# Kernel optimization log

Hardware: AMD Instinct MI355X
Metric: run time of the kernel (lower is better)

## Reference

```python
import jax, jax.numpy as jnp
import numpy as np

HEAD_DIM = 64
SELECT = 256  # number of selected rows/cols (m)
NUM_ITER = 4  # Newton-Schulz iterations


def _select_idx(T, mask, m):
    # top-k over sum of features (select_type='sum'), done under stop_gradient (torch.no_grad)
    somme = jax.lax.stop_gradient(jnp.sum(T, axis=-1))  # [B,H,N]
    neg = -jnp.finfo(somme.dtype).max
    somme = jnp.where(mask[:, None, :], somme, neg)
    _, idx = jax.lax.top_k(somme, m)  # [B,H,m], descending like argsort(descending=True)[:m]
    return idx


def _gather_rows(T, idx):
    # T: [B,H,N,D], idx: [B,H,m] -> [B,H,m,D]  (index_select over flattened (b h n))
    return jnp.take_along_axis(T, idx[..., None], axis=2)


def _iterative_inv(mat, num_iter):
    m = mat.shape[-1]
    I = jnp.eye(m, dtype=mat.dtype)
    K = mat
    # V0 = K^T / max_j(sum_i K_ij)
    scale = 1.0 / jnp.max(jnp.sum(K, axis=-2), axis=-1)[:, :, None, None]
    V = scale * jnp.swapaxes(K, -1, -2)
    for _ in range(num_iter):
        KV = jnp.matmul(K, V)
        V = jnp.matmul(0.25 * V, 13.0 * I - jnp.matmul(KV, 15.0 * I - jnp.matmul(KV, 7.0 * I - KV)))
    return V


def setup_inputs() -> dict:
    key = jax.random.key(0)
    kq, kk, kv = jax.random.split(key, 3)
    B, H, N, D = 2, 8, 4096, HEAD_DIM
    Q = jax.random.normal(kq, (B, H, N, D), dtype=jnp.float32)
    K = jax.random.normal(kk, (B, H, N, D), dtype=jnp.float32)
    V = jax.random.normal(kv, (B, H, N, D), dtype=jnp.float32)
    mask = jnp.ones((B, N), dtype=bool)
    return {"Q": Q, "K": K, "V": V, "mask": mask}


def reference(Q, K, V, mask):
    m = SELECT
    Qs = Q / np.sqrt(HEAD_DIM).astype(np.float32)
    # select_mode='default' -> index_select_different: indices for K from K, for Q from (scaled) Q
    idx_k = _select_idx(K, mask, m)
    idx_q = _select_idx(Qs, mask, m)
    nc = _gather_rows(K, idx_k)   # [B,H,m,D] selected columns (from K)
    nr = _gather_rows(Qs, idx_k := idx_q if False else idx_q) if False else _gather_rows(Qs, idx_q)  # [B,H,m,D]
    c = jnp.einsum('bhnd,bhmd->bhnm', Qs, nc)   # [B,H,N,m]
    r = jnp.einsum('bhmd,bhnd->bhmn', nr, K)    # [B,H,m,N]
    neg = -jnp.finfo(Qs.dtype).max
    r = jnp.where(mask[:, None, None, :], r, neg)
    kernel_1 = jax.nn.softmax(c, axis=-1)                 # [B,H,N,m]
    u = _gather_rows(kernel_1, idx_q)                     # [B,H,m,m]
    kernel_3 = jax.nn.softmax(r, axis=-1)                 # [B,H,m,N]
    kernel_2_inv = _iterative_inv(u, NUM_ITER)            # [B,H,m,m]
    RV = jnp.matmul(kernel_3, V)                          # [B,H,m,D]
    X = jnp.matmul(kernel_1, jnp.matmul(kernel_2_inv, RV))  # [B,H,N,D]
    return X
```

## Files before the change

### kernel.cpp

```cpp
#include <hip/hip_runtime.h>
#include <float.h>


#define G    16
#define NSEQ 4096
#define DH   64
#define MSEL 256
#define NSL  16

typedef __attribute__((ext_vector_type(8))) short short8;
typedef __attribute__((ext_vector_type(4))) float floatx4;
typedef __attribute__((ext_vector_type(4))) unsigned short ushort4v;
typedef unsigned short ush;

static __device__ __forceinline__ ush f2b(float x) {
    union { float f; unsigned u; } c{x};
    unsigned r = c.u + 0x7FFFu + ((c.u >> 16) & 1u);
    return (ush)(r >> 16);
}
static __device__ __forceinline__ float b2f(ush h) {
    union { unsigned u; float f; } c{(unsigned)h << 16};
    return c.f;
}
static __device__ __forceinline__ void split_store(ush* __restrict__ h, ush* __restrict__ l,
                                                   int off, float4 v, float scale) {
    float a0 = v.x * scale, a1 = v.y * scale, a2 = v.z * scale, a3 = v.w * scale;
    ush h0 = f2b(a0), h1 = f2b(a1), h2 = f2b(a2), h3 = f2b(a3);
    ushort4v hv = { h0, h1, h2, h3 };
    ushort4v lv = { f2b(a0 - b2f(h0)), f2b(a1 - b2f(h1)), f2b(a2 - b2f(h2)), f2b(a3 - b2f(h3)) };
    *(ushort4v*)&h[off] = hv;
    *(ushort4v*)&l[off] = lv;
}
static __device__ __forceinline__ floatx4 mfma3(short8 ah, short8 al, short8 bh, short8 bl, floatx4 acc) {
    acc = __builtin_amdgcn_mfma_f32_16x16x32_bf16(al, bh, acc, 0, 0, 0);
    acc = __builtin_amdgcn_mfma_f32_16x16x32_bf16(ah, bl, acc, 0, 0, 0);
    acc = __builtin_amdgcn_mfma_f32_16x16x32_bf16(ah, bh, acc, 0, 0, 0);
    return acc;
}

__global__ __launch_bounds__(256) void rowsum_kernel(const float* __restrict__ Q, const float* __restrict__ K,
                                                     float* __restrict__ sumQ, float* __restrict__ sumK,
                                                     float* __restrict__ k2) {
    long row = (long)blockIdx.x * 16 + (threadIdx.x >> 4);
    int c4 = (threadIdx.x & 15) * 4;
    float4 q = *(const float4*)(Q + row * DH + c4);
    float4 k = *(const float4*)(K + row * DH + c4);
    float qs = q.x + q.y + q.z + q.w;
    float ks = k.x + k.y + k.z + k.w;
    float k2s = k.x * k.x + k.y * k.y + k.z * k.z + k.w * k.w;
#pragma unroll
    for (int off = 8; off; off >>= 1) {
        qs += __shfl_xor(qs, off); ks += __shfl_xor(ks, off); k2s += __shfl_xor(k2s, off);
    }
    if ((threadIdx.x & 15) == 0) { sumQ[row] = qs; sumK[row] = ks; k2[row] = k2s; }
}

__global__ __launch_bounds__(256) void topk_select(const float* __restrict__ sumQ, const float* __restrict__ sumK,
                                                   int* __restrict__ idxQ, int* __restrict__ idxK,
                                                   const float* __restrict__ k2, float* __restrict__ Kmax2,
                                                   float* __restrict__ colsum) {
    __shared__ unsigned red[4];
    __shared__ float redf[4];
    __shared__ unsigned eqpre[64];
    __shared__ unsigned cnt_sel;
    int g = blockIdx.x, which = blockIdx.y;
    const float* s = (which ? sumK : sumQ) + (long)g * NSEQ;
    int* out = (which ? idxK : idxQ) + g * MSEL;
    int t = threadIdx.x, lane = t & 63, wid = t >> 6;
    if (which == 0) colsum[g * 256 + t] = 0.f;
    unsigned k[16];
#pragma unroll
    for (int i = 0; i < 16; i++) {
        unsigned u = __float_as_uint(s[t + 256 * i]);
        k[i] = (u & 0x80000000u) ? ~u : (u | 0x80000000u);
    }
    unsigned T = 0;
    for (int b = 31; b >= 0; b--) {
        unsigned trial = T | (1u << b);
        int c = 0;
#pragma unroll
        for (int i = 0; i < 16; i++) c += (k[i] >= trial);
#pragma unroll
        for (int off = 32; off; off >>= 1) c += __shfl_xor(c, off);
        __syncthreads();
        if (lane == 0) red[wid] = (unsigned)c;
        __syncthreads();
        unsigned tot = red[0] + red[1] + red[2] + red[3];
        if (tot == MSEL) { T = trial; break; }
        if (tot > MSEL) T = trial;
    }
    int cg = 0;
#pragma unroll
    for (int i = 0; i < 16; i++) cg += (k[i] > T);
#pragma unroll
    for (int off = 32; off; off >>= 1) cg += __shfl_xor(cg, off);
    __syncthreads();
    if (lane == 0) red[wid] = (unsigned)cg;
    if (t == 0) cnt_sel = 0;
    __syncthreads();
    unsigned ngreater = red[0] + red[1] + red[2] + red[3];
    unsigned want_eq = MSEL - ngreater;
#pragma unroll
    for (int i = 0; i < 16; i++) {
        unsigned long long be = __ballot(k[i] == T);
        if (lane == 0) eqpre[i * 4 + wid] = (unsigned)__popcll(be);
    }
    __syncthreads();
    if (t == 0) {
        unsigned run = 0;
        for (int j = 0; j < 64; j++) { unsigned c = eqpre[j]; eqpre[j] = run; run += c; }
    }
    __syncthreads();
#pragma unroll
    for (int i = 0; i < 16; i++) {
        int idx = t + 256 * i;
        unsigned long long lt = (1ull << lane) - 1;
        bool gt = (k[i] > T);
        unsigned long long bg = __ballot(gt);
        unsigned wbase = 0;
        if (lane == 0) wbase = atomicAdd(&cnt_sel, (unsigned)__popcll(bg));
        wbase = __shfl((int)wbase, 0);
        if (gt) out[wbase + __popcll(bg & lt)] = idx;
        bool eq = (k[i] == T);
        unsigned long long be = __ballot(eq);
        if (eq) {
            unsigned rank = eqpre[i * 4 + wid] + (unsigned)__popcll(be & lt);
            if (rank < want_eq) out[ngreater + rank] = idx;
        }
    }
    if (which == 1) {
        float mx = 0.f;
#pragma unroll
        for (int i = 0; i < 16; i++) mx = fmaxf(mx, k2[(long)g * NSEQ + t + 256 * i]);
#pragma unroll
        for (int off = 32; off; off >>= 1) mx = fmaxf(mx, __shfl_xor(mx, off));
        __syncthreads();
        if (lane == 0) redf[wid] = mx;
        __syncthreads();
        if (t == 0) Kmax2[g] = fmaxf(fmaxf(redf[0], redf[1]), fmaxf(redf[2], redf[3]));
    }
}

__global__ __launch_bounds__(256) void gather_kernel(const float* __restrict__ Q, const float* __restrict__ K,
                                                     const int* __restrict__ idxQ, const int* __restrict__ idxK,
                                                     const float* __restrict__ Kmax2,
                                                     float* __restrict__ nr,
                                                     ush* __restrict__ ncH, ush* __restrict__ ncL,
                                                     float* __restrict__ Mb) {
    int wid = threadIdx.x >> 6, lane = threadIdx.x & 63;
    long t = (long)blockIdx.x * 4 + wid;
    long g = t >> 8;
    int iq = idxQ[t], ik = idxK[t];
    float qv = Q[(g * NSEQ + iq) * DH + lane] * 0.125f;
    nr[t * DH + lane] = qv;
    float kv = K[(g * NSEQ + ik) * DH + lane];
    ush h = f2b(kv);
    ncH[t * DH + lane] = h;
    ncL[t * DH + lane] = f2b(kv - b2f(h));
    float n2 = qv * qv;
#pragma unroll
    for (int off = 32; off; off >>= 1) n2 += __shfl_xor(n2, off);
    if (lane == 0) Mb[t] = sqrtf(n2 * Kmax2[g]);
}

__global__ __launch_bounds__(256, 4) void flash_rv(const float* __restrict__ nr, const float* __restrict__ K,
                                                   const float* __restrict__ V, const float* __restrict__ Mb,
                                                   float* __restrict__ Lp, float* __restrict__ RVp) {
    __shared__ __align__(16) ush B1h[64 * 72];
    __shared__ __align__(16) ush B1l[64 * 72];
    __shared__ __align__(16) ush Ph[64 * 72];
    __shared__ float msh[64];
    __shared__ float lred[64][2];
    int ns = blockIdx.x, s = blockIdx.y, g = blockIdx.z;
    int t = threadIdx.x, lane = t & 63, w = t >> 6;
    int wr = w >> 1, wc = w & 1, ml = lane & 15, quad = lane >> 4;
    int lr = t >> 2, lq = t & 3;
    const float* nrg = nr + (long)g * 16384 + (long)s * 64 * 64;
    const float* Kg  = K + (long)g * 262144 + (long)ns * 256 * 64;
    const float* Vg  = V + (long)g * 262144 + (long)ns * 256 * 64;
    short8 Ah[2][2], Al[2][2];
#pragma unroll
    for (int i2 = 0; i2 < 2; i2++)
#pragma unroll
        for (int kq = 0; kq < 2; kq++) {
            const float* p = nrg + (wr * 32 + i2 * 16 + ml) * 64 + kq * 32 + quad * 8;
            float4 f0 = *(const float4*)p;
            float4 f1 = *(const float4*)(p + 4);
            float vals[8] = { f0.x, f0.y, f0.z, f0.w, f1.x, f1.y, f1.z, f1.w };
            short8 hh, ll;
#pragma unroll
            for (int j = 0; j < 8; j++) {
                ush h = f2b(vals[j]);
                hh[j] = (short)h;
                ll[j] = (short)f2b(vals[j] - b2f(h));
            }
            Ah[i2][kq] = hh; Al[i2][kq] = ll;
        }
    if (t < 64) msh[t] = Mb[g * 256 + s * 64 + t];
    float lsum[2][4] = {};
    floatx4 acc[2][2] = {};
    int vn = t >> 2, vdq = (t & 3) * 16;
    for (int it = 0; it < 4; it++) {
        __syncthreads();
        float4 kv[4], vv[4];
#pragma unroll
        for (int q = 0; q < 4; q++) kv[q] = *(const float4*)(Kg + (long)(it * 64 + lr) * 64 + lq * 16 + q * 4);
#pragma unroll
        for (int q = 0; q < 4; q++) vv[q] = *(const float4*)(Vg + (long)(it * 64 + vn) * 64 + vdq + q * 4);
#pragma unroll
        for (int q = 0; q < 4; q++) split_store(B1h, B1l, lr * 72 + lq * 16 + q * 4, kv[q], 1.0f);
        __syncthreads();
        floatx4 sa[2][2] = {};
#pragma unroll
        for (int kq = 0; kq < 2; kq++) {
            short8 b0h = *(const short8*)&B1h[(wc * 32 + ml) * 72 + kq * 32 + quad * 8];
            short8 b0l = *(const short8*)&B1l[(wc * 32 + ml) * 72 + kq * 32 + quad * 8];
            short8 b1h = *(const short8*)&B1h[(wc * 32 + 16 + ml) * 72 + kq * 32 + quad * 8];
            short8 b1l = *(const short8*)&B1l[(wc * 32 + 16 + ml) * 72 + kq * 32 + quad * 8];
            sa[0][0] = mfma3(Ah[0][kq], Al[0][kq], b0h, b0l, sa[0][0]);
            sa[0][1] = mfma3(Ah[0][kq], Al[0][kq], b1h, b1l, sa[0][1]);
            sa[1][0] = mfma3(Ah[1][kq], Al[1][kq], b0h, b0l, sa[1][0]);
            sa[1][1] = mfma3(Ah[1][kq], Al[1][kq], b1h, b1l, sa[1][1]);
        }
        __syncthreads();
#pragma unroll
        for (int i2 = 0; i2 < 2; i2++)
#pragma unroll
            for (int r = 0; r < 4; r++) {
                int row = wr * 32 + i2 * 16 + quad * 4 + r;
                float M = msh[row];
                float p0 = __expf(sa[i2][0][r] - M);
                float p1 = __expf(sa[i2][1][r] - M);
                lsum[i2][r] += p0 + p1;
                Ph[row * 72 + wc * 32 + ml] = f2b(p0);
                Ph[row * 72 + wc * 32 + 16 + ml] = f2b(p1);
            }
#pragma unroll
        for (int q = 0; q < 4; q++)
#pragma unroll
            for (int c = 0; c < 4; c++) {
                int d = vdq + q * 4 + c;
                int addr = d * 72 + ((((vn >> 3) ^ ((d >> 4) & 3)) << 3) | (vn & 7));
                B1h[addr] = f2b((&vv[q].x)[c]);
            }
        __syncthreads();
#pragma unroll
        for (int kq = 0; kq < 2; kq++) {
            short8 a0 = *(const short8*)&Ph[(wr * 32 + ml) * 72 + kq * 32 + quad * 8];
            short8 a1 = *(const short8*)&Ph[(wr * 32 + 16 + ml) * 72 + kq * 32 + quad * 8];
            int nb = kq * 4 + quad;
            short8 b0 = *(const short8*)&B1h[(wc * 32 + ml) * 72 + ((nb ^ (2 * wc)) << 3)];
            short8 b1 = *(const short8*)&B1h[(wc * 32 + 16 + ml) * 72 + ((nb ^ (2 * wc + 1)) << 3)];
            acc[0][0] = __builtin_amdgcn_mfma_f32_16x16x32_bf16(a0, b0, acc[0][0], 0, 0, 0);
            acc[0][1] = __builtin_amdgcn_mfma_f32_16x16x32_bf16(a0, b1, acc[0][1], 0, 0, 0);
            acc[1][0] = __builtin_amdgcn_mfma_f32_16x16x32_bf16(a1, b0, acc[1][0], 0, 0, 0);
            acc[1][1] = __builtin_amdgcn_mfma_f32_16x16x32_bf16(a1, b1, acc[1][1], 0, 0, 0);
        }
    }
#pragma unroll
    for (int i2 = 0; i2 < 2; i2++)
#pragma unroll
        for (int r = 0; r < 4; r++) {
            float v = lsum[i2][r];
#pragma unroll
            for (int off = 8; off; off >>= 1) v += __shfl_xor(v, off);
            if (ml == 0) lred[wr * 32 + i2 * 16 + quad * 4 + r][wc] = v;
        }
    __syncthreads();
    long p = ((long)(g * 4 + s)) * NSL + ns;
    if (t < 64) Lp[p * 64 + t] = lred[t][0] + lred[t][1];
    float* rvp = RVp + p * 4096;
#pragma unroll
    for (int i2 = 0; i2 < 2; i2++)
#pragma unroll
        for (int j2 = 0; j2 < 2; j2++)
#pragma unroll
            for (int r = 0; r < 4; r++)
                rvp[(wr * 32 + i2 * 16 + quad * 4 + r) * 64 + wc * 32 + j2 * 16 + ml] = acc[i2][j2][r];
}

template <int MODE>
__global__ __launch_bounds__(256, 4) void fused_cx(const float* __restrict__ A,
                                                   const ush* __restrict__ ncH, const ush* __restrict__ ncL,
                                                   const ush* __restrict__ WtH, const ush* __restrict__ WtL,
                                                   float* __restrict__ Out, float* __restrict__ colsum,
                                                   float ascale) {
    __shared__ __align__(16) ush SM[18432];
    ush* Ah = SM;            ush* Al = SM + 4608;
    ush* Bh = SM + 9216;     ush* Bl = SM + 13824;
    ush* Ph = SM;            ush* Pl = SM + 4608;
    ush* Wh = SM + 9216;     ush* Wl = SM + 13824;
    __shared__ float pm[256], ps[256], Mr[64], Lr[64];
    int strip = blockIdx.x, g = blockIdx.y;
    int t = threadIdx.x, lane = t & 63, w = t >> 6;
    int wr = w >> 1, wc = w & 1, ml = lane & 15, quad = lane >> 4;
    int lr = t >> 2, lq = t & 3;
    long aRows = (MODE == 0) ? 4096 : 256;
    const float* Ag = A + (long)g * aRows * 64 + (long)strip * 64 * 64;
    const ush* ncHg = ncH + (long)g * 16384;
    const ush* ncLg = ncL + (long)g * 16384;
#pragma unroll
    for (int q = 0; q < 4; q++) {
        float4 v = *(const float4*)(Ag + lr * 64 + lq * 16 + q * 4);
        split_store(Ah, Al, lr * 72 + lq * 16 + q * 4, v, ascale);
    }
    floatx4 sacc[4][4] = {};
    for (int c = 0; c < 4; c++) {
        __syncthreads();
        {
            const ush* sH = ncHg + (c * 64 + lr) * 64;
            const ush* sL = ncLg + (c * 64 + lr) * 64;
            *(uint4*)&Bh[lr * 72 + lq * 8]       = *(const uint4*)&sH[lq * 8];
            *(uint4*)&Bh[lr * 72 + (lq + 4) * 8] = *(const uint4*)&sH[(lq + 4) * 8];
            *(uint4*)&Bl[lr * 72 + lq * 8]       = *(const uint4*)&sL[lq * 8];
            *(uint4*)&Bl[lr * 72 + (lq + 4) * 8] = *(const uint4*)&sL[(lq + 4) * 8];
        }
        __syncthreads();
#pragma unroll
        for (int kq = 0; kq < 2; kq++) {
            short8 bh = *(const short8*)&Bh[(w * 16 + ml) * 72 + kq * 32 + quad * 8];
            short8 bl = *(const short8*)&Bl[(w * 16 + ml) * 72 + kq * 32 + quad * 8];
#pragma unroll
            for (int i = 0; i < 4; i++) {
                short8 afh = *(const short8*)&Ah[(16 * i + ml) * 72 + kq * 32 + quad * 8];
                short8 afl = *(const short8*)&Al[(16 * i + ml) * 72 + kq * 32 + quad * 8];
                sacc[c][i] = mfma3(afh, afl, bh, bl, sacc[c][i]);
            }
        }
    }
#pragma unroll
    for (int i = 0; i < 4; i++)
#pragma unroll
        for (int r = 0; r < 4; r++) {
            float mx = fmaxf(fmaxf(sacc[0][i][r], sacc[1][i][r]), fmaxf(sacc[2][i][r], sacc[3][i][r]));
#pragma unroll
            for (int off = 8; off; off >>= 1) mx = fmaxf(mx, __shfl_xor(mx, off));
            if (ml == 0) pm[(16 * i + quad * 4 + r) * 4 + w] = mx;
        }
    __syncthreads();
    if (t < 64) Mr[t] = fmaxf(fmaxf(pm[t * 4], pm[t * 4 + 1]), fmaxf(pm[t * 4 + 2], pm[t * 4 + 3]));
    __syncthreads();
#pragma unroll
    for (int i = 0; i < 4; i++)
#pragma unroll
        for (int r = 0; r < 4; r++) {
            int row = 16 * i + quad * 4 + r;
            float M = Mr[row];
            float sum = 0.f;
#pragma unroll
            for (int c = 0; c < 4; c++) {
                float p = __expf(sacc[c][i][r] - M);
                sacc[c][i][r] = p;
                sum += p;
            }
#pragma unroll
            for (int off = 8; off; off >>= 1) sum += __shfl_xor(sum, off);
            if (ml == 0) ps[row * 4 + w] = sum;
        }
    __syncthreads();
    if (t < 64) Lr[t] = ps[t * 4] + ps[t * 4 + 1] + ps[t * 4 + 2] + ps[t * 4 + 3];
    __syncthreads();
    if (MODE == 1) {
        float invL[4][4];
#pragma unroll
        for (int i = 0; i < 4; i++)
#pragma unroll
            for (int r = 0; r < 4; r++) invL[i][r] = 1.0f / Lr[16 * i + quad * 4 + r];
        float* ug = Out + (long)g * 65536 + (long)strip * 64 * 256;
#pragma unroll
        for (int i = 0; i < 4; i++)
#pragma unroll
            for (int r = 0; r < 4; r++) {
                int row = 16 * i + quad * 4 + r;
#pragma unroll
                for (int c = 0; c < 4; c++)
                    ug[(long)row * 256 + c * 64 + w * 16 + ml] = sacc[c][i][r] * invL[i][r];
            }
#pragma unroll
        for (int c = 0; c < 4; c++) {
            float v = 0.f;
#pragma unroll
            for (int i = 0; i < 4; i++)
#pragma unroll
                for (int r = 0; r < 4; r++) v += sacc[c][i][r] * invL[i][r];
            v += __shfl_xor(v, 16);
            v += __shfl_xor(v, 32);
            if (quad == 0) atomicAdd(&colsum[g * 256 + c * 64 + w * 16 + ml], v);
        }
        return;
    }
    floatx4 xacc[2][2] = {};
    const ush* wHg = WtH + (long)g * 16384;
    const ush* wLg = WtL + (long)g * 16384;
#pragma unroll
    for (int h = 0; h < 4; h++) {
        __syncthreads();
#pragma unroll
        for (int i = 0; i < 4; i++)
#pragma unroll
            for (int r = 0; r < 4; r++) {
                int row = 16 * i + quad * 4 + r;
                float p = sacc[h][i][r];
                ush hh = f2b(p);
                Ph[row * 72 + w * 16 + ml] = hh;
                Pl[row * 72 + w * 16 + ml] = f2b(p - b2f(hh));
            }
        {
            const ush* sH = wHg + lr * 256 + h * 64;
            const ush* sL = wLg + lr * 256 + h * 64;
            *(uint4*)&Wh[lr * 72 + lq * 8]       = *(const uint4*)&sH[lq * 8];
            *(uint4*)&Wh[lr * 72 + (lq + 4) * 8] = *(const uint4*)&sH[(lq + 4) * 8];
            *(uint4*)&Wl[lr * 72 + lq * 8]       = *(const uint4*)&sL[lq * 8];
            *(uint4*)&Wl[lr * 72 + (lq + 4) * 8] = *(const uint4*)&sL[(lq + 4) * 8];
        }
        __syncthreads();
#pragma unroll
        for (int kq = 0; kq < 2; kq++) {
            short8 a0h = *(const short8*)&Ph[(wr * 32 + ml) * 72 + kq * 32 + quad * 8];
            short8 a0l = *(const short8*)&Pl[(wr * 32 + ml) * 72 + kq * 32 + quad * 8];
            short8 a1h = *(const short8*)&Ph[(wr * 32 + 16 + ml) * 72 + kq * 32 + quad * 8];
            short8 a1l = *(const short8*)&Pl[(wr * 32 + 16 + ml) * 72 + kq * 32 + quad * 8];
            short8 b0h = *(const short8*)&Wh[(wc * 32 + ml) * 72 + kq * 32 + quad * 8];
            short8 b0l = *(const short8*)&Wl[(wc * 32 + ml) * 72 + kq * 32 + quad * 8];
            short8 b1h = *(const short8*)&Wh[(wc * 32 + 16 + ml) * 72 + kq * 32 + quad * 8];
            short8 b1l = *(const short8*)&Wl[(wc * 32 + 16 + ml) * 72 + kq * 32 + quad * 8];
            xacc[0][0] = mfma3(a0h, a0l, b0h, b0l, xacc[0][0]);
            xacc[0][1] = mfma3(a0h, a0l, b1h, b1l, xacc[0][1]);
            xacc[1][0] = mfma3(a1h, a1l, b0h, b0l, xacc[1][0]);
            xacc[1][1] = mfma3(a1h, a1l, b1h, b1l, xacc[1][1]);
        }
    }
    float* outg = Out + (long)g * 262144 + (long)strip * 64 * 64;
#pragma unroll
    for (int i2 = 0; i2 < 2; i2++)
#pragma unroll
        for (int j2 = 0; j2 < 2; j2++)
#pragma unroll
            for (int r = 0; r < 4; r++) {
                int row = wr * 32 + i2 * 16 + quad * 4 + r;
                outg[(long)row * 64 + wc * 32 + j2 * 16 + ml] = xacc[i2][j2][r] / Lr[row];
            }
}

__global__ __launch_bounds__(256) void mergeprep_kernel(const float* __restrict__ Lp, const float* __restrict__ RVp,
                                                        ush* __restrict__ RVt,
                                                        const float* __restrict__ u, const float* __restrict__ colsum,
                                                        ush* __restrict__ u_bf, ush* __restrict__ V0,
                                                        float* __restrict__ scale) {
    __shared__ float tile[64][65];
    __shared__ float smax[4];
    int g = blockIdx.y;
    int t = threadIdx.x, lane = t & 63, wid = t >> 6;
    if (blockIdx.z == 0) {
        int s = blockIdx.x >> 2, mq = blockIdx.x & 3;
        int d = t & 63;
        int m0 = mq * 16 + (t >> 6) * 4;
        long pb = ((long)(g * 4 + s)) * NSL;
#pragma unroll
        for (int mm = 0; mm < 4; mm++) {
            int rho = m0 + mm;
            float L = 0.f, val = 0.f;
#pragma unroll
            for (int n = 0; n < NSL; n++) {
                L   += Lp[(pb + n) * 64 + rho];
                val += RVp[(pb + n) * 4096 + rho * 64 + d];
            }
            RVt[(long)g * 16384 + d * 256 + s * 64 + rho] = f2b(val / L);
        }
        return;
    }
    int tc = blockIdx.x & 3, tr = (blockIdx.x >> 2) & 3;
    float v = colsum[g * 256 + t];
#pragma unroll
    for (int off = 32; off; off >>= 1) v = fmaxf(v, __shfl_xor(v, off));
    if (lane == 0) smax[wid] = v;
    __syncthreads();
    float sc = 1.0f / fmaxf(fmaxf(smax[0], smax[1]), fmaxf(smax[2], smax[3]));
    if (t == 0 && tr == 0 && tc == 0) scale[g] = sc;
    long base = (long)g * MSEL * MSEL;
    const float* ug = u + base;
    int cq = (t & 15) * 4, r0 = t >> 4;
#pragma unroll
    for (int i = 0; i < 4; i++) {
        int r = r0 + 16 * i;
        float4 vv = *(const float4*)&ug[(long)(tr * 64 + r) * MSEL + tc * 64 + cq];
        long o = base + (long)(tr * 64 + r) * MSEL + tc * 64 + cq;
        ushort4v ub = { f2b(vv.x), f2b(vv.y), f2b(vv.z), f2b(vv.w) };
        *(ushort4v*)&u_bf[o] = ub;
        tile[r][cq] = vv.x; tile[r][cq + 1] = vv.y; tile[r][cq + 2] = vv.z; tile[r][cq + 3] = vv.w;
    }
    __syncthreads();
#pragma unroll
    for (int i = 0; i < 4; i++) {
        int r = r0 + 16 * i;
        ushort4v o = { f2b(sc * tile[cq][r]), f2b(sc * tile[cq + 1][r]),
                       f2b(sc * tile[cq + 2][r]), f2b(sc * tile[cq + 3][r]) };
        *(ushort4v*)&V0[base + (long)(tc * 64 + r) * MSEL + tr * 64 + cq] = o;
    }
}

__global__ __launch_bounds__(256) void nsAC(const ush* __restrict__ A0, const ush* __restrict__ B0t,
                                            const ush* __restrict__ A1, const ush* __restrict__ B1t,
                                            ush* __restrict__ C0rm, ush* __restrict__ C0t,
                                            ush* __restrict__ C1rm,
                                            const float* __restrict__ scale, int whichBase) {
    const int LD = 136;
    __shared__ __align__(16) ush As[64 * LD];
    __shared__ __align__(16) ush Bs[64 * LD];
    int z = blockIdx.z, g = z & 15, which = (z >> 4) + whichBase;
    int tm = blockIdx.y, tn = blockIdx.x;
    long base = (long)g * 65536;
    const ush* Ag = (which ? A1 : A0) + base + (long)tm * 64 * 256;
    const ush* Bg = (which ? B1t : B0t) + base + (long)tn * 64 * 256;
    int t = threadIdx.x;
    int lr = t >> 2, lq = t & 3;
    int w = t >> 6, lane = t & 63;
    int wr = w >> 1, wc = w & 1;
    int ml = lane & 15, quad = lane >> 4;
    floatx4 acc[2][2] = {};
#pragma unroll
    for (int h = 0; h < 2; h++) {
        __syncthreads();
#pragma unroll
        for (int rr = 0; rr < 4; rr++) {
            int col = (lq + 4 * rr) * 8;
            *(uint4*)&As[lr * LD + col] = *(const uint4*)(Ag + lr * 256 + h * 128 + col);
            *(uint4*)&Bs[lr * LD + col] = *(const uint4*)(Bg + lr * 256 + h * 128 + col);
        }
        __syncthreads();
#pragma unroll
        for (int kq = 0; kq < 4; kq++) {
            int ko = kq * 32 + quad * 8;
            short8 a0 = *(const short8*)&As[(wr * 32 + ml) * LD + ko];
            short8 a1 = *(const short8*)&As[(wr * 32 + 16 + ml) * LD + ko];
            short8 b0 = *(const short8*)&Bs[(wc * 32 + ml) * LD + ko];
            short8 b1 = *(const short8*)&Bs[(wc * 32 + 16 + ml) * LD + ko];
            acc[0][0] = __builtin_amdgcn_mfma_f32_16x16x32_bf16(a0, b0, acc[0][0], 0, 0, 0);
            acc[0][1] = __builtin_amdgcn_mfma_f32_16x16x32_bf16(a0, b1, acc[0][1], 0, 0, 0);
            acc[1][0] = __builtin_amdgcn_mfma_f32_16x16x32_bf16(a1, b0, acc[1][0], 0, 0, 0);
            acc[1][1] = __builtin_amdgcn_mfma_f32_16x16x32_bf16(a1, b1, acc[1][1], 0, 0, 0);
        }
    }
    float sc = (which == 0 && scale) ? scale[g] : 1.0f;
    int rowb = tm * 64 + wr * 32, colb = tn * 64 + wc * 32;
#pragma unroll
    for (int i = 0; i < 2; i++) {
#pragma unroll
        for (int j = 0; j < 2; j++) {
            int col = colb + j * 16 + ml;
            int r0 = rowb + i * 16 + quad * 4;
            ush h[4];
#pragma unroll
            for (int r = 0; r < 4; r++) h[r] = f2b(acc[i][j][r] * sc);
            if (which == 0) {
#pragma unroll
                for (int r = 0; r < 4; r++) C0rm[base + (long)(r0 + r) * 256 + col] = h[r];
                ushort4v ht = { h[0], h[1], h[2], h[3] };
                *(ushort4v*)&C0t[base + (long)col * 256 + r0] = ht;
            } else {
#pragma unroll
                for (int r = 0; r < 4; r++) C1rm[base + (long)(r0 + r) * 256 + col] = h[r];
            }
        }
    }
}

template <bool FINAL>
__global__ __launch_bounds__(256) void nsB(const ush* __restrict__ S, const ush* __restrict__ Et,
                                           const ush* __restrict__ St,
                                           ush* __restrict__ Eo, ush* __restrict__ Eot,
                                           ush* __restrict__ Pt) {
    const int LD = 136;
    __shared__ __align__(16) ush As[64 * LD];
    __shared__ __align__(16) ush B1s[64 * LD];
    __shared__ __align__(16) ush B2s[64 * LD];
    int g = blockIdx.z, tm = blockIdx.y, tn = blockIdx.x;
    long base = (long)g * 65536;
    const ush* Ag  = S + base + (long)tm * 64 * 256;
    const ush* B1g = Et + base + (long)tn * 64 * 256;
    const ush* B2g = St + base + (long)tn * 64 * 256;
    int t = threadIdx.x;
    int lr = t >> 2, lq = t & 3;
    int w = t >> 6, lane = t & 63;
    int wr = w >> 1, wc = w & 1;
    int ml = lane & 15, quad = lane >> 4;
    floatx4 acc1[2][2] = {};
    floatx4 acc2[2][2] = {};
#pragma unroll
    for (int h = 0; h < 2; h++) {
        __syncthreads();
#pragma unroll
        for (int rr = 0; rr < 4; rr++) {
            int col = (lq + 4 * rr) * 8;
            *(uint4*)&As[lr * LD + col]  = *(const uint4*)(Ag + lr * 256 + h * 128 + col);
            *(uint4*)&B1s[lr * LD + col] = *(const uint4*)(B1g + lr * 256 + h * 128 + col);
            if (!FINAL) *(uint4*)&B2s[lr * LD + col] = *(const uint4*)(B2g + lr * 256 + h * 128 + col);
        }
        __syncthreads();
#pragma unroll
        for (int kq = 0; kq < 4; kq++) {
            int ko = kq * 32 + quad * 8;
            short8 a0 = *(const short8*)&As[(wr * 32 + ml) * LD + ko];
            short8 a1 = *(const short8*)&As[(wr * 32 + 16 + ml) * LD + ko];
            short8 b10 = *(const short8*)&B1s[(wc * 32 + ml) * LD + ko];
            short8 b11 = *(const short8*)&B1s[(wc * 32 + 16 + ml) * LD + ko];
            acc1[0][0] = __builtin_amdgcn_mfma_f32_16x16x32_bf16(a0, b10, acc1[0][0], 0, 0, 0);
            acc1[0][1] = __builtin_amdgcn_mfma_f32_16x16x32_bf16(a0, b11, acc1[0][1], 0, 0, 0);
            acc1[1][0] = __builtin_amdgcn_mfma_f32_16x16x32_bf16(a1, b10, acc1[1][0], 0, 0, 0);
            acc1[1][1] = __builtin_amdgcn_mfma_f32_16x16x32_bf16(a1, b11, acc1[1][1], 0, 0, 0);
            if (!FINAL) {
                short8 b20 = *(const short8*)&B2s[(wc * 32 + ml) * LD + ko];
                short8 b21 = *(const short8*)&B2s[(wc * 32 + 16 + ml) * LD + ko];
                acc2[0][0] = __builtin_amdgcn_mfma_f32_16x16x32_bf16(a0, b20, acc2[0][0], 0, 0, 0);
                acc2[0][1] = __builtin_amdgcn_mfma_f32_16x16x32_bf16(a0, b21, acc2[0][1], 0, 0, 0);
                acc2[1][0] = __builtin_amdgcn_mfma_f32_16x16x32_bf16(a1, b20, acc2[1][0], 0, 0, 0);
                acc2[1][1] = __builtin_amdgcn_mfma_f32_16x16x32_bf16(a1, b21, acc2[1][1], 0, 0, 0);
            }
        }
    }
    int rowb = tm * 64 + wr * 32, colb = tn * 64 + wc * 32;
#pragma unroll
    for (int i = 0; i < 2; i++) {
#pragma unroll
        for (int j = 0; j < 2; j++) {
            int col = colb + j * 16 + ml;
            int r0 = rowb + i * 16 + quad * 4;
            ushort4v et = *(const ushort4v*)&Et[base + (long)col * 256 + r0];
            ushort4v st = *(const ushort4v*)&St[base + (long)col * 256 + r0];
            ushort4v pv;
#pragma unroll
            for (int r = 0; r < 4; r++) {
                float e = b2f(et[r]), s = b2f(st[r]);
                float p = 0.25f * (((r0 + r == col) ? 13.0f : 0.0f) - 15.0f * e + 7.0f * s - acc1[i][j][r]);
                pv[r] = f2b(p);
            }
            *(ushort4v*)&Pt[base + (long)col * 256 + r0] = pv;
            if (!FINAL) {
                ush h[4];
#pragma unroll
                for (int r = 0; r < 4; r++) {
                    float e = b2f(et[r]), s = b2f(st[r]);
                    float en = 0.25f * (13.0f * e - 15.0f * s + 7.0f * acc1[i][j][r] - acc2[i][j][r]);
                    h[r] = f2b(en);
                }
#pragma unroll
                for (int r = 0; r < 4; r++) Eo[base + (long)(r0 + r) * 256 + col] = h[r];
                ushort4v ht = { h[0], h[1], h[2], h[3] };
                *(ushort4v*)&Eot[base + (long)col * 256 + r0] = ht;
            }
        }
    }
}

__global__ __launch_bounds__(256) void nsW(const ush* __restrict__ V4, const ush* __restrict__ RVt,
                                           ush* __restrict__ WtH, ush* __restrict__ WtL) {
    const int LD = 136;
    __shared__ __align__(16) ush As[64 * LD];
    __shared__ __align__(16) ush Bs[64 * LD];
    int g = blockIdx.z, tm = blockIdx.y;
    long base = (long)g * 65536;
    const ush* Ag = V4 + base + (long)tm * 64 * 256;
    const ush* Bg = RVt + (long)g * 16384;
    int t = threadIdx.x;
    int lr = t >> 2, lq = t & 3;
    int w = t >> 6, lane = t & 63;
    int wr = w >> 1, wc = w & 1;
    int ml = lane & 15, quad = lane >> 4;
    floatx4 acc[2][2] = {};
#pragma unroll
    for (int h = 0; h < 2; h++) {
        __syncthreads();
#pragma unroll
        for (int rr = 0; rr < 4; rr++) {
            int col = (lq + 4 * rr) * 8;
            *(uint4*)&As[lr * LD + col] = *(const uint4*)(Ag + lr * 256 + h * 128 + col);
            *(uint4*)&Bs[lr * LD + col] = *(const uint4*)(Bg + lr * 256 + h * 128 + col);
        }
        __syncthreads();
#pragma unroll
        for (int kq = 0; kq < 4; kq++) {
            int ko = kq * 32 + quad * 8;
            short8 a0 = *(const short8*)&As[(wr * 32 + ml) * LD + ko];
            short8 a1 = *(const short8*)&As[(wr * 32 + 16 + ml) * LD + ko];
            short8 b0 = *(const short8*)&Bs[(wc * 32 + ml) * LD + ko];
            short8 b1 = *(const short8*)&Bs[(wc * 32 + 16 + ml) * LD + ko];
            acc[0][0] = __builtin_amdgcn_mfma_f32_16x16x32_bf16(a0, b0, acc[0][0], 0, 0, 0);
            acc[0][1] = __builtin_amdgcn_mfma_f32_16x16x32_bf16(a0, b1, acc[0][1], 0, 0, 0);
            acc[1][0] = __builtin_amdgcn_mfma_f32_16x16x32_bf16(a1, b0, acc[1][0], 0, 0, 0);
            acc[1][1] = __builtin_amdgcn_mfma_f32_16x16x32_bf16(a1, b1, acc[1][1], 0, 0, 0);
        }
    }
    int rowb = tm * 64 + wr * 32, colb = wc * 32;
#pragma unroll
    for (int i = 0; i < 2; i++) {
#pragma unroll
        for (int j = 0; j < 2; j++) {
            int col = colb + j * 16 + ml;
            int r0 = rowb + i * 16 + quad * 4;
            ushort4v hv, lv;
#pragma unroll
            for (int r = 0; r < 4; r++) {
                float v = acc[i][j][r];
                ush h = f2b(v);
                hv[r] = h;
                lv[r] = f2b(v - b2f(h));
            }
            *(ushort4v*)&WtH[(long)g * 16384 + (long)col * 256 + r0] = hv;
            *(ushort4v*)&WtL[(long)g * 16384 + (long)col * 256 + r0] = lv;
        }
    }
}

extern "C" void kernel_launch(void* const* d_in, const int* in_sizes, int n_in,
                              void* d_out, int out_size, void* d_ws, size_t ws_size,
                              hipStream_t stream) {
    (void)in_sizes; (void)n_in; (void)out_size; (void)ws_size;
    const float* Q = (const float*)d_in[0];
    const float* K = (const float*)d_in[1];
    const float* V = (const float*)d_in[2];

    float* ws    = (float*)d_ws;
    float* sumQ  = ws;
    float* sumK  = sumQ + 65536;
    float* k2    = sumK + 65536;
    float* nr    = k2 + 65536;
    float* u     = nr + 262144;
    float* Mb    = u + 1048576;
    float* Kmax2 = Mb + 4096;
    float* scale = Kmax2 + 16;
    float* colsum= scale + 16 + 32;
    float* Lp    = colsum + 4096;
    float* RVp   = Lp + 65536;
    int* idxQ    = (int*)(RVp + 4194304);
    int* idxK    = idxQ + 4096;
    ush* ncH     = (ush*)(idxK + 4096);
    ush* ncL     = ncH + 262144;
    ush* WtH     = ncL + 262144;
    ush* WtL     = WtH + 262144;
    ush* RVt     = WtL + 262144;
    ush* u_bf    = RVt + 262144;
    ush* Vacc_a  = u_bf + 1048576;
    ush* Vacc_b  = Vacc_a + 1048576;
    ush* E_a     = Vacc_b + 1048576;
    ush* Et_a    = E_a + 1048576;
    ush* E_b     = Et_a + 1048576;
    ush* Et_b    = E_b + 1048576;
    ush* Sbuf    = Et_b + 1048576;
    ush* St      = Sbuf + 1048576;
    ush* Ptb     = St + 1048576;

    dim3 blk(256);

    hipLaunchKernelGGL(rowsum_kernel, dim3(G * NSEQ / 16), blk, 0, stream, Q, K, sumQ, sumK, k2);
    hipLaunchKernelGGL(topk_select, dim3(G, 2), blk, 0, stream, sumQ, sumK, idxQ, idxK, k2, Kmax2, colsum);
    hipLaunchKernelGGL(gather_kernel, dim3(G * MSEL / 4), blk, 0, stream, Q, K, idxQ, idxK, Kmax2, nr, ncH, ncL, Mb);

    hipLaunchKernelGGL(flash_rv, dim3(NSL, 4, G), blk, 0, stream, nr, K, V, Mb, Lp, RVp);

    hipLaunchKernelGGL((fused_cx<1>), dim3(4, G), blk, 0, stream, nr, ncH, ncL,
                       (const ush*)0, (const ush*)0, u, colsum, 1.0f);

    hipLaunchKernelGGL(mergeprep_kernel, dim3(16, G, 2), blk, 0, stream,
                       Lp, RVp, RVt, u, colsum, u_bf, Vacc_a, scale);

    hipLaunchKernelGGL(nsAC, dim3(4, 4, G), blk, 0, stream,
                       u_bf, u_bf, (const ush*)0, (const ush*)0, E_a, Et_a, (ush*)0, scale, 0);
    hipLaunchKernelGGL(nsAC, dim3(4, 4, G), blk, 0, stream,
                       E_a, Et_a, (const ush*)0, (const ush*)0, Sbuf, St, (ush*)0, (const float*)0, 0);

    ush* E = E_a;  ush* Et = Et_a;
    ush* En = E_b; ush* Ent = Et_b;
    ush* Vc = Vacc_a; ush* Vn = Vacc_b;
    for (int i = 0; i < 3; i++) {
        hipLaunchKernelGGL((nsB<false>), dim3(4, 4, G), blk, 0, stream, Sbuf, Et, St, En, Ent, Ptb);
        hipLaunchKernelGGL(nsAC, dim3(4, 4, 2 * G), blk, 0, stream,
                           En, Ent, Vc, Ptb, Sbuf, St, Vn, (const float*)0, 0);
        ush* tp;
        tp = E; E = En; En = tp;
        tp = Et; Et = Ent; Ent = tp;
        tp = Vc; Vc = Vn; Vn = tp;
    }
    hipLaunchKernelGGL((nsB<true>), dim3(4, 4, G), blk, 0, stream, Sbuf, Et, St, (ush*)0, (ush*)0, Ptb);
    hipLaunchKernelGGL(nsAC, dim3(4, 4, G), blk, 0, stream,
                       (const ush*)0, (const ush*)0, Vc, Ptb, (ush*)0, (ush*)0, Vn, (const float*)0, 1);
    hipLaunchKernelGGL(nsW, dim3(1, 4, G), blk, 0, stream, Vn, RVt, WtH, WtL);

    hipLaunchKernelGGL((fused_cx<0>), dim3(64, G), blk, 0, stream, Q, ncH, ncL, WtH, WtL,
                       (float*)d_out, (float*)0, 0.125f);
}
```

Baseline: 255.3 us.

## Fuse gather into top-k and merge cx1 softmax into flash_rv launch

The top-k kernel now keeps the selected indices in shared memory and performs the Q/K row gather and bf16 hi/lo split itself, removing the separate gather kernel and the index round trip. The per-row bound Mb is recomputed inside the flash kernel from the loaded nr rows. The fused_cx<1> u-matrix softmax work runs as an extra block column (blockIdx.x == NSL) of the flash kernel. Together these drop two launches and let the u computation overlap with the flash pass. The cost is a gather done by only 32 blocks, which limits memory parallelism, and a larger shared-memory footprint per flash block.

```diff
diff --git a/kernel.cpp b/kernel.cpp
--- a/kernel.cpp
+++ b/kernel.cpp
@@ -55,17 +55,19 @@
     if ((threadIdx.x & 15) == 0) { sumQ[row] = qs; sumK[row] = ks; k2[row] = k2s; }
 }
 
-__global__ __launch_bounds__(256) void topk_select(const float* __restrict__ sumQ, const float* __restrict__ sumK,
-                                                   int* __restrict__ idxQ, int* __restrict__ idxK,
+__global__ __launch_bounds__(256) void topk_gather(const float* __restrict__ Q, const float* __restrict__ K,
+                                                   const float* __restrict__ sumQ, const float* __restrict__ sumK,
                                                    const float* __restrict__ k2, float* __restrict__ Kmax2,
-                                                   float* __restrict__ colsum) {
+                                                   float* __restrict__ colsum,
+                                                   float* __restrict__ nr,
+                                                   ush* __restrict__ ncH, ush* __restrict__ ncL) {
     __shared__ unsigned red[4];
     __shared__ float redf[4];
     __shared__ unsigned eqpre[64];
     __shared__ unsigned cnt_sel;
+    __shared__ int sel[MSEL];
     int g = blockIdx.x, which = blockIdx.y;
     const float* s = (which ? sumK : sumQ) + (long)g * NSEQ;
-    int* out = (which ? idxK : idxQ) + g * MSEL;
     int t = threadIdx.x, lane = t & 63, wid = t >> 6;
     if (which == 0) colsum[g * 256 + t] = 0.f;
     unsigned k[16];
@@ -120,12 +122,12 @@
         unsigned wbase = 0;
         if (lane == 0) wbase = atomicAdd(&cnt_sel, (unsigned)__popcll(bg));
         wbase = __shfl((int)wbase, 0);
-        if (gt) out[wbase + __popcll(bg & lt)] = idx;
+        if (gt) sel[wbase + __popcll(bg & lt)] = idx;
         bool eq = (k[i] == T);
         unsigned long long be = __ballot(eq);
         if (eq) {
             unsigned rank = eqpre[i * 4 + wid] + (unsigned)__popcll(be & lt);
-            if (rank < want_eq) out[ngreater + rank] = idx;
+            if (rank < want_eq) sel[ngreater + rank] = idx;
         }
     }
     if (which == 1) {
@@ -139,46 +141,163 @@
         __syncthreads();
         if (t == 0) Kmax2[g] = fmaxf(fmaxf(redf[0], redf[1]), fmaxf(redf[2], redf[3]));
     }
-}
-
-__global__ __launch_bounds__(256) void gather_kernel(const float* __restrict__ Q, const float* __restrict__ K,
-                                                     const int* __restrict__ idxQ, const int* __restrict__ idxK,
-                                                     const float* __restrict__ Kmax2,
-                                                     float* __restrict__ nr,
-                                                     ush* __restrict__ ncH, ush* __restrict__ ncL,
-                                                     float* __restrict__ Mb) {
-    int wid = threadIdx.x >> 6, lane = threadIdx.x & 63;
-    long t = (long)blockIdx.x * 4 + wid;
-    long g = t >> 8;
-    int iq = idxQ[t], ik = idxK[t];
-    float qv = Q[(g * NSEQ + iq) * DH + lane] * 0.125f;
-    nr[t * DH + lane] = qv;
-    float kv = K[(g * NSEQ + ik) * DH + lane];
-    ush h = f2b(kv);
-    ncH[t * DH + lane] = h;
-    ncL[t * DH + lane] = f2b(kv - b2f(h));
-    float n2 = qv * qv;
-#pragma unroll
-    for (int off = 32; off; off >>= 1) n2 += __shfl_xor(n2, off);
-    if (lane == 0) Mb[t] = sqrtf(n2 * Kmax2[g]);
-}
-
-__global__ __launch_bounds__(256, 4) void flash_rv(const float* __restrict__ nr, const float* __restrict__ K,
-                                                   const float* __restrict__ V, const float* __restrict__ Mb,
-                                                   float* __restrict__ Lp, float* __restrict__ RVp) {
-    __shared__ __align__(16) ush B1h[64 * 72];
-    __shared__ __align__(16) ush B1l[64 * 72];
-    __shared__ __align__(16) ush Ph[64 * 72];
-    __shared__ float msh[64];
-    __shared__ float lred[64][2];
-    int ns = blockIdx.x, s = blockIdx.y, g = blockIdx.z;
+    __syncthreads();
+    int i0 = t >> 2, cq = (t & 3) * 16;
+    if (which == 0) {
+        const float* Qg = Q + (long)g * NSEQ * DH;
+        float* nrg = nr + (long)g * MSEL * DH;
+#pragma unroll
+        for (int rr = 0; rr < 4; rr++) {
+            int i = rr * 64 + i0;
+            long row = sel[i];
+#pragma unroll
+            for (int q = 0; q < 4; q++) {
+                float4 v = *(const float4*)(Qg + row * DH + cq + q * 4);
+                v.x *= 0.125f; v.y *= 0.125f; v.z *= 0.125f; v.w *= 0.125f;
+                *(float4*)(nrg + (long)i * DH + cq + q * 4) = v;
+            }
+        }
+    } else {
+        const float* Kg = K + (long)g * NSEQ * DH;
+        ush* hH = ncH + (long)g * MSEL * DH;
+        ush* hL = ncL + (long)g * MSEL * DH;
+#pragma unroll
+        for (int rr = 0; rr < 4; rr++) {
+            int i = rr * 64 + i0;
+            long row = sel[i];
+#pragma unroll
+            for (int q = 0; q < 4; q++) {
+                float4 v = *(const float4*)(Kg + row * DH + cq + q * 4);
+                split_store(hH, hL, i * DH + cq + q * 4, v, 1.0f);
+            }
+        }
+    }
+}
+
+__global__ __launch_bounds__(256, 4) void flash_cx1(const float* __restrict__ nr, const float* __restrict__ K,
+                                                    const float* __restrict__ V, const float* __restrict__ Kmax2,
+                                                    float* __restrict__ Lp, float* __restrict__ RVp,
+                                                    const ush* __restrict__ ncH, const ush* __restrict__ ncL,
+                                                    float* __restrict__ u, float* __restrict__ colsum) {
+    __shared__ __align__(16) unsigned char SMEM[39424];
     int t = threadIdx.x, lane = t & 63, w = t >> 6;
     int wr = w >> 1, wc = w & 1, ml = lane & 15, quad = lane >> 4;
     int lr = t >> 2, lq = t & 3;
+    int g = blockIdx.z;
+
+    if (blockIdx.x == NSL) {
+        ush* Ah = (ush*)SMEM;            ush* Al = (ush*)(SMEM + 9216);
+        ush* Bh = (ush*)(SMEM + 18432);  ush* Bl = (ush*)(SMEM + 27648);
+        float* pm = (float*)(SMEM + 36864);
+        float* ps = pm + 256;
+        float* Mr = ps + 256;
+        float* Lr = Mr + 64;
+        int strip = blockIdx.y;
+        const float* Ag = nr + (long)g * 256 * 64 + (long)strip * 64 * 64;
+        const ush* ncHg = ncH + (long)g * 16384;
+        const ush* ncLg = ncL + (long)g * 16384;
+#pragma unroll
+        for (int q = 0; q < 4; q++) {
+            float4 v = *(const float4*)(Ag + lr * 64 + lq * 16 + q * 4);
+            split_store(Ah, Al, lr * 72 + lq * 16 + q * 4, v, 1.0f);
+        }
+        floatx4 sacc[4][4] = {};
+        for (int c = 0; c < 4; c++) {
+            __syncthreads();
+            {
+                const ush* sH = ncHg + (c * 64 + lr) * 64;
+                const ush* sL = ncLg + (c * 64 + lr) * 64;
+                *(uint4*)&Bh[lr * 72 + lq * 8]       = *(const uint4*)&sH[lq * 8];
+                *(uint4*)&Bh[lr * 72 + (lq + 4) * 8] = *(const uint4*)&sH[(lq + 4) * 8];
+                *(uint4*)&Bl[lr * 72 + lq * 8]       = *(const uint4*)&sL[lq * 8];
+                *(uint4*)&Bl[lr * 72 + (lq + 4) * 8] = *(const uint4*)&sL[(lq + 4) * 8];
+            }
+            __syncthreads();
+#pragma unroll
+            for (int kq = 0; kq < 2; kq++) {
+                short8 bh = *(const short8*)&Bh[(w * 16 + ml) * 72 + kq * 32 + quad * 8];
+                short8 bl = *(const short8*)&Bl[(w * 16 + ml) * 72 + kq * 32 + quad * 8];
+#pragma unroll
+                for (int i = 0; i < 4; i++) {
+                    short8 afh = *(const short8*)&Ah[(16 * i + ml) * 72 + kq * 32 + quad * 8];
+                    short8 afl = *(const short8*)&Al[(16 * i + ml) * 72 + kq * 32 + quad * 8];
+                    sacc[c][i] = mfma3(afh, afl, bh, bl, sacc[c][i]);
+                }
+            }
+        }
+#pragma unroll
+        for (int i = 0; i < 4; i++)
+#pragma unroll
+            for (int r = 0; r < 4; r++) {
+                float mx = fmaxf(fmaxf(sacc[0][i][r], sacc[1][i][r]), fmaxf(sacc[2][i][r], sacc[3][i][r]));
+#pragma unroll
+                for (int off = 8; off; off >>= 1) mx = fmaxf(mx, __shfl_xor(mx, off));
+                if (ml == 0) pm[(16 * i + quad * 4 + r) * 4 + w] = mx;
+            }
+        __syncthreads();
+        if (t < 64) Mr[t] = fmaxf(fmaxf(pm[t * 4], pm[t * 4 + 1]), fmaxf(pm[t * 4 + 2], pm[t * 4 + 3]));
+        __syncthreads();
+#pragma unroll
+        for (int i = 0; i < 4; i++)
+#pragma unroll
+            for (int r = 0; r < 4; r++) {
+                int row = 16 * i + quad * 4 + r;
+                float M = Mr[row];
+                float sum = 0.f;
+#pragma unroll
+                for (int c = 0; c < 4; c++) {
+                    float p = __expf(sacc[c][i][r] - M);
+                    sacc[c][i][r] = p;
+                    sum += p;
+                }
+#pragma unroll
+                for (int off = 8; off; off >>= 1) sum += __shfl_xor(sum, off);
+                if (ml == 0) ps[row * 4 + w] = sum;
+            }
+        __syncthreads();
+        if (t < 64) Lr[t] = ps[t * 4] + ps[t * 4 + 1] + ps[t * 4 + 2] + ps[t * 4 + 3];
+        __syncthreads();
+        float invL[4][4];
+#pragma unroll
+        for (int i = 0; i < 4; i++)
+#pragma unroll
+            for (int r = 0; r < 4; r++) invL[i][r] = 1.0f / Lr[16 * i + quad * 4 + r];
+        float* ug = u + (long)g * 65536 + (long)strip * 64 * 256;
+#pragma unroll
+        for (int i = 0; i < 4; i++)
+#pragma unroll
+            for (int r = 0; r < 4; r++) {
+                int row = 16 * i + quad * 4 + r;
+#pragma unroll
+                for (int c = 0; c < 4; c++)
+                    ug[(long)row * 256 + c * 64 + w * 16 + ml] = sacc[c][i][r] * invL[i][r];
+            }
+#pragma unroll
+        for (int c = 0; c < 4; c++) {
+            float v = 0.f;
+#pragma unroll
+            for (int i = 0; i < 4; i++)
+#pragma unroll
+                for (int r = 0; r < 4; r++) v += sacc[c][i][r] * invL[i][r];
+            v += __shfl_xor(v, 16);
+            v += __shfl_xor(v, 32);
+            if (quad == 0) atomicAdd(&colsum[g * 256 + c * 64 + w * 16 + ml], v);
+        }
+        return;
+    }
+
+    ush* B1h = (ush*)SMEM;
+    ush* B1l = (ush*)(SMEM + 9216);
+    ush* Ph  = (ush*)(SMEM + 18432);
+    float* msh  = (float*)(SMEM + 27648);
+    float* lred = msh + 64;
+    int ns = blockIdx.x, s = blockIdx.y;
     const float* nrg = nr + (long)g * 16384 + (long)s * 64 * 64;
     const float* Kg  = K + (long)g * 262144 + (long)ns * 256 * 64;
     const float* Vg  = V + (long)g * 262144 + (long)ns * 256 * 64;
+    float km2 = Kmax2[g];
     short8 Ah[2][2], Al[2][2];
+    float s2[2] = { 0.f, 0.f };
 #pragma unroll
     for (int i2 = 0; i2 < 2; i2++)
 #pragma unroll
@@ -190,13 +309,20 @@
             short8 hh, ll;
 #pragma unroll
             for (int j = 0; j < 8; j++) {
+                s2[i2] += vals[j] * vals[j];
                 ush h = f2b(vals[j]);
                 hh[j] = (short)h;
                 ll[j] = (short)f2b(vals[j] - b2f(h));
             }
             Ah[i2][kq] = hh; Al[i2][kq] = ll;
         }
-    if (t < 64) msh[t] = Mb[g * 256 + s * 64 + t];
+#pragma unroll
+    for (int i2 = 0; i2 < 2; i2++) {
+        float v = s2[i2];
+        v += __shfl_xor(v, 16);
+        v += __shfl_xor(v, 32);
+        if (quad == 0) msh[wr * 32 + i2 * 16 + ml] = sqrtf(v * km2);
+    }
     float lsum[2][4] = {};
     floatx4 acc[2][2] = {};
     int vn = t >> 2, vdq = (t & 3) * 16;
@@ -264,11 +390,11 @@
             float v = lsum[i2][r];
 #pragma unroll
             for (int off = 8; off; off >>= 1) v += __shfl_xor(v, off);
-            if (ml == 0) lred[wr * 32 + i2 * 16 + quad * 4 + r][wc] = v;
+            if (ml == 0) lred[(wr * 32 + i2 * 16 + quad * 4 + r) * 2 + wc] = v;
         }
     __syncthreads();
     long p = ((long)(g * 4 + s)) * NSL + ns;
-    if (t < 64) Lp[p * 64 + t] = lred[t][0] + lred[t][1];
+    if (t < 64) Lp[p * 64 + t] = lred[t * 2] + lred[t * 2 + 1];
     float* rvp = RVp + p * 4096;
 #pragma unroll
     for (int i2 = 0; i2 < 2; i2++)
@@ -361,32 +487,6 @@
     if (t < 64) Lr[t] = ps[t * 4] + ps[t * 4 + 1] + ps[t * 4 + 2] + ps[t * 4 + 3];
     __syncthreads();
     if (MODE == 1) {
-        float invL[4][4];
-#pragma unroll
-        for (int i = 0; i < 4; i++)
-#pragma unroll
-            for (int r = 0; r < 4; r++) invL[i][r] = 1.0f / Lr[16 * i + quad * 4 + r];
-        float* ug = Out + (long)g * 65536 + (long)strip * 64 * 256;
-#pragma unroll
-        for (int i = 0; i < 4; i++)
-#pragma unroll
-            for (int r = 0; r < 4; r++) {
-                int row = 16 * i + quad * 4 + r;
-#pragma unroll
-                for (int c = 0; c < 4; c++)
-                    ug[(long)row * 256 + c * 64 + w * 16 + ml] = sacc[c][i][r] * invL[i][r];
-            }
-#pragma unroll
-        for (int c = 0; c < 4; c++) {
-            float v = 0.f;
-#pragma unroll
-            for (int i = 0; i < 4; i++)
-#pragma unroll
-                for (int r = 0; r < 4; r++) v += sacc[c][i][r] * invL[i][r];
-            v += __shfl_xor(v, 16);
-            v += __shfl_xor(v, 32);
-            if (quad == 0) atomicAdd(&colsum[g * 256 + c * 64 + w * 16 + ml], v);
-        }
         return;
     }
     floatx4 xacc[2][2] = {};
@@ -752,13 +852,11 @@
     dim3 blk(256);
 
     hipLaunchKernelGGL(rowsum_kernel, dim3(G * NSEQ / 16), blk, 0, stream, Q, K, sumQ, sumK, k2);
-    hipLaunchKernelGGL(topk_select, dim3(G, 2), blk, 0, stream, sumQ, sumK, idxQ, idxK, k2, Kmax2, colsum);
-    hipLaunchKernelGGL(gather_kernel, dim3(G * MSEL / 4), blk, 0, stream, Q, K, idxQ, idxK, Kmax2, nr, ncH, ncL, Mb);
-
-    hipLaunchKernelGGL(flash_rv, dim3(NSL, 4, G), blk, 0, stream, nr, K, V, Mb, Lp, RVp);
-
-    hipLaunchKernelGGL((fused_cx<1>), dim3(4, G), blk, 0, stream, nr, ncH, ncL,
-                       (const ush*)0, (const ush*)0, u, colsum, 1.0f);
+    hipLaunchKernelGGL(topk_gather, dim3(G, 2), blk, 0, stream,
+                       Q, K, sumQ, sumK, k2, Kmax2, colsum, nr, ncH, ncL);
+
+    hipLaunchKernelGGL(flash_cx1, dim3(NSL + 1, 4, G), blk, 0, stream,
+                       nr, K, V, Kmax2, Lp, RVp, ncH, ncL, u, colsum);
 
     hipLaunchKernelGGL(mergeprep_kernel, dim3(16, G, 2), blk, 0, stream,
                        Lp, RVp, RVt, u, colsum, u_bf, Vacc_a, scale);
```

Result: no change. 258.0 us (+1.0%).
